# Kernel tuning notes

Measured on AMD Instinct MI355X. Metric: run time of the kernel, lower is better.

The kernel has to match this reference:

```python
import jax, jax.numpy as jnp
import numpy as np

EPS = 1e-3
D_MODEL = 512
SEQ = 1024
BATCH = 4
N_LAYERS = 2
N_HEAD = 8
D_HEAD = 64
D_INNER = 1024


def _position_table(n_pos, d):
    # Faithful to PositionEncoding: sin applied to even cols; the cos line in
    # the source is a no-op (missing assignment), so odd cols stay raw.
    j = np.arange(d)
    pos = np.arange(n_pos)[:, None]
    pe = pos / np.power(10000.0, 2 * (j // 2) / d)
    pe[0] = 0.0
    pe[1:, 0::2] = np.sin(pe[1:, 0::2])
    return jnp.asarray(pe, dtype=jnp.float32)


def _layer_norm(z, a, b):
    # torch.std is unbiased (ddof=1); eps added to sigma, not variance
    mu = jnp.mean(z, axis=-1, keepdims=True)
    sigma = jnp.sqrt(jnp.sum((z - mu) ** 2, axis=-1, keepdims=True) / (z.shape[-1] - 1))
    return (z - mu) / (sigma + EPS) * a + b


def setup_inputs() -> dict:
    key = jax.random.key(0)
    ks = jax.random.split(key, 10)
    s = 0.02
    return {
        "x": jax.random.normal(ks[0], (BATCH, SEQ, D_MODEL), dtype=jnp.float32),
        "pos_enc": _position_table(SEQ, D_MODEL),
        "w_qs": jax.random.normal(ks[1], (N_LAYERS, N_HEAD, D_MODEL, D_HEAD), dtype=jnp.float32) * s,
        "w_ks": jax.random.normal(ks[2], (N_LAYERS, N_HEAD, D_MODEL, D_HEAD), dtype=jnp.float32) * s,
        "w_vs": jax.random.normal(ks[3], (N_LAYERS, N_HEAD, D_MODEL, D_HEAD), dtype=jnp.float32) * s,
        "ln1_a": jnp.ones((N_LAYERS, D_MODEL), dtype=jnp.float32),
        "ln1_b": jnp.zeros((N_LAYERS, D_MODEL), dtype=jnp.float32),
        "w1": jax.random.normal(ks[4], (N_LAYERS, D_INNER, D_MODEL), dtype=jnp.float32) * s,
        "b1": jax.random.normal(ks[5], (N_LAYERS, D_INNER), dtype=jnp.float32) * s,
        "w2": jax.random.normal(ks[6], (N_LAYERS, D_MODEL, D_INNER), dtype=jnp.float32) * s,
        "b2": jax.random.normal(ks[7], (N_LAYERS, D_MODEL), dtype=jnp.float32) * s,
        "ln2_a": jnp.ones((N_LAYERS, D_MODEL), dtype=jnp.float32),
        "ln2_b": jnp.zeros((N_LAYERS, D_MODEL), dtype=jnp.float32),
    }


def reference(x, pos_enc, w_qs, w_ks, w_vs, ln1_a, ln1_b, w1, b1, w2, b2, ln2_a, ln2_b):
    temper = jnp.sqrt(jnp.float32(D_MODEL))  # scale uses d_model, not d_k (as in source)
    x = x + pos_enc[None, :, :]
    for i in range(N_LAYERS):
        residual = x
        # per-head projections: [h, b, l, dk]
        q = jnp.einsum('bld,hdk->hblk', x, w_qs[i])
        k = jnp.einsum('bld,hdk->hblk', x, w_ks[i])
        v = jnp.einsum('bld,hdv->hblv', x, w_vs[i])
        attn = jax.nn.softmax(jnp.einsum('hbqk,hbmk->hbqm', q, k) / temper, axis=-1)
        out = jnp.einsum('hbqm,hbmv->hbqv', attn, v)
        # permute(1,2,0,3): concat heads along feature dim -> [b, l, h*dv]
        out = out.transpose(1, 2, 0, 3).reshape(BATCH, SEQ, N_HEAD * D_HEAD)
        x = _layer_norm(out + residual, ln1_a[i], ln1_b[i])
        # positionwise FFN (1x1 convs == linears)
        h = jax.nn.relu(jnp.einsum('bld,fd->blf', x, w1[i]) + b1[i])
        o = jnp.einsum('blf,df->bld', h, w2[i]) + b2[i]
        x = _layer_norm(o + x, ln2_a[i], ln2_b[i])
    return x
```

## Files before the change

kernel.cpp:

```cpp
#include <hip/hip_runtime.h>
#include <math.h>

#define D_MODEL 512
#define SEQ     1024
#define BATCH   4
#define N_LAYERS 2
#define N_HEAD  8
#define D_HEAD  64
#define D_INNER 1024
#define NTOK    (BATCH*SEQ)
#define LN_EPS  1e-3f

typedef float f32x4 __attribute__((ext_vector_type(4)));
typedef short bf16x8 __attribute__((ext_vector_type(8)));
typedef unsigned short ushort_t;
typedef unsigned int uint_t;
typedef unsigned long long ull_t;

__device__ inline ushort_t f2bf(float f) {
    uint_t u = __float_as_uint(f);
    u += 0x7FFFu + ((u >> 16) & 1u);
    return (ushort_t)(u >> 16);
}
__device__ inline float bf2f(ushort_t h) {
    return __uint_as_float((uint_t)h << 16);
}

#define PREP_E0 (NTOK * D_MODEL)
#define PREP_E1 (1536 * 512)
#define PREP_EW (N_LAYERS * D_INNER * D_MODEL)
#define PREP_TOTAL (PREP_E0 + 2 * PREP_E1 + 2 * PREP_EW)

__global__ void prep_kernel(const float* __restrict__ x,
                            const float* __restrict__ pe,
                            const float* __restrict__ w_qs,
                            const float* __restrict__ w_ks,
                            const float* __restrict__ w_vs,
                            const float* __restrict__ w1,
                            const float* __restrict__ w2,
                            float* __restrict__ X,
                            ushort_t* __restrict__ Xraw,
                            ushort_t* __restrict__ Wqkv,
                            ushort_t* __restrict__ WqkvL,
                            ushort_t* __restrict__ W1b,
                            ushort_t* __restrict__ W2b) {
    int idx = blockIdx.x * 256 + threadIdx.x;
    if (idx < PREP_E0) {
        int l = (idx / D_MODEL) % SEQ;
        int d = idx % D_MODEL;
        float xv = x[idx];
        X[idx] = xv + pe[l * D_MODEL + d];
        Xraw[idx] = f2bf(xv);
        return;
    }
    idx -= PREP_E0;
    if (idx < 2 * PREP_E1) {
        int layer = idx / PREP_E1;
        int j = idx - layer * PREP_E1;
        int n = j >> 9, k = j & 511;
        int which = n >> 9, h = (n >> 6) & 7, d = n & 63;
        size_t wofs = (size_t)layer * N_HEAD * D_MODEL * D_HEAD;
        const float* W = (which == 0) ? w_qs + wofs
                       : (which == 1) ? w_ks + wofs : w_vs + wofs;
        float v = W[((size_t)h * D_MODEL + k) * D_HEAD + d];
        ushort_t hv = f2bf(v);
        Wqkv[(size_t)layer * PREP_E1 + j] = hv;
        if (layer == 0) WqkvL[j] = f2bf(v - bf2f(hv));
        return;
    }
    idx -= 2 * PREP_E1;
    if (idx < PREP_EW) { W1b[idx] = f2bf(w1[idx]); return; }
    idx -= PREP_EW;
    W2b[idx] = f2bf(w2[idx]);
}

__device__ inline void qkv_scatter(f32x4 a, int n, int m_base,
                                   const float* __restrict__ pew,
                                   ushort_t* Qhi, ushort_t* Qlo,
                                   ushort_t* Khi, ushort_t* Klo,
                                   ushort_t* Vt) {
    int which = n >> 9, hd = n & 511;
    int head = hd >> 6, d = hd & 63;
    int hb = head * BATCH + (m_base >> 10);
    int l  = m_base & 1023;
    if (pew) {
#pragma unroll
        for (int r = 0; r < 4; r++) a[r] += pew[(size_t)(l + r) * 1536 + n];
    }
    if (which == 2) {
        ushort4 pk = make_ushort4(f2bf(a[0]), f2bf(a[1]), f2bf(a[2]), f2bf(a[3]));
        *(ushort4*)(Vt + ((size_t)hb * D_HEAD + d) * SEQ + l) = pk;
    } else {
        ushort_t* H = (which == 0) ? Qhi : Khi;
        ushort_t* L = (which == 0) ? Qlo : Klo;
#pragma unroll
        for (int r = 0; r < 4; r++) {
            float v = a[r];
            ushort_t hv = f2bf(v);
            size_t off = ((size_t)hb * SEQ + l + r) * D_HEAD + d;
            H[off] = hv;
            L[off] = f2bf(v - bf2f(hv));
        }
    }
}

template<int MODE, int TM, int TN, int BK>
__global__ __launch_bounds__(256, 4)
void gemm_kernel(const ushort_t* __restrict__ A, const ushort_t* __restrict__ Bt,
                 const float* __restrict__ bias, const float* __restrict__ pew,
                 float* __restrict__ outF, ushort_t* __restrict__ outB,
                 ushort_t* __restrict__ Qhi, ushort_t* __restrict__ Qlo,
                 ushort_t* __restrict__ Khi, ushort_t* __restrict__ Klo,
                 ushort_t* __restrict__ Vt,
                 int M, int N, int K) {
    constexpr int WM = TM / 2, WN = TN / 2;
    constexpr int MT = WM / 16, NT = WN / 16;
    constexpr int CPR = BK / 8;
    __shared__ ushort_t As[TM][BK + 8];
    __shared__ ushort_t Bs[TN][BK + 8];
    const int tid = threadIdx.x;
    const int m0 = blockIdx.y * TM, n0 = blockIdx.x * TN;
    const int w = tid >> 6, lane = tid & 63;
    const int wr = w >> 1, wc = w & 1;
    const int col = lane & 15, quad = lane >> 4;

    f32x4 acc[MT][NT] = {};

    for (int k0 = 0; k0 < K; k0 += BK) {
        __syncthreads();
#pragma unroll
        for (int p = 0; p < TM * CPR / 256; p++) {
            int idx = p * 256 + tid;
            int row = idx / CPR, ch = (idx % CPR) * 8;
            *(uint4*)(&As[row][ch]) =
                *(const uint4*)(A + (size_t)(m0 + row) * K + k0 + ch);
        }
#pragma unroll
        for (int p = 0; p < TN * CPR / 256; p++) {
            int idx = p * 256 + tid;
            int row = idx / CPR, ch = (idx % CPR) * 8;
            *(uint4*)(&Bs[row][ch]) =
                *(const uint4*)(Bt + (size_t)(n0 + row) * K + k0 + ch);
        }
        __syncthreads();
#pragma unroll
        for (int ks = 0; ks < BK; ks += 32) {
            bf16x8 af[MT], bfr[NT];
#pragma unroll
            for (int t = 0; t < MT; t++)
                af[t] = *(const bf16x8*)(&As[wr * WM + t * 16 + col][ks + quad * 8]);
#pragma unroll
            for (int t = 0; t < NT; t++)
                bfr[t] = *(const bf16x8*)(&Bs[wc * WN + t * 16 + col][ks + quad * 8]);
#pragma unroll
            for (int mt = 0; mt < MT; mt++)
#pragma unroll
                for (int nt = 0; nt < NT; nt++)
                    acc[mt][nt] = __builtin_amdgcn_mfma_f32_16x16x32_bf16(
                        af[mt], bfr[nt], acc[mt][nt], 0, 0, 0);
        }
    }

#pragma unroll
    for (int mt = 0; mt < MT; mt++) {
#pragma unroll
        for (int nt = 0; nt < NT; nt++) {
            int n = n0 + wc * WN + nt * 16 + col;
            int m_base = m0 + wr * WM + mt * 16 + quad * 4;
            if (MODE == 0) {
                qkv_scatter(acc[mt][nt], n, m_base, pew, Qhi, Qlo, Khi, Klo, Vt);
            } else {
#pragma unroll
                for (int r = 0; r < 4; r++) {
                    int m = m_base + r;
                    float v = acc[mt][nt][r];
                    if (MODE == 1) {
                        float t = fmaxf(v + bias[n], 0.f);
                        outB[(size_t)m * N + n] = f2bf(t);
                    } else {
                        outF[(size_t)m * N + n] = v + bias[n];
                    }
                }
            }
        }
    }
}

__global__ __launch_bounds__(256, 4)
void gemm_hilo_kernel(const float* __restrict__ A,
                      const ushort_t* __restrict__ Bh,
                      const ushort_t* __restrict__ Bl,
                      float* __restrict__ outF, int M, int N, int K) {
    __shared__ ushort_t Ash[64][72];
    __shared__ ushort_t Asl[64][72];
    __shared__ ushort_t Bsh[64][72];
    __shared__ ushort_t Bsl[64][72];
    const int tid = threadIdx.x;
    const int m0 = blockIdx.y * 64, n0 = blockIdx.x * 64;
    const int w = tid >> 6, lane = tid & 63;
    const int wm = (w >> 1) * 32, wn = (w & 1) * 32;
    const int col = lane & 15, quad = lane >> 4;

    f32x4 acc[2][2] = {};

    for (int k0 = 0; k0 < K; k0 += 64) {
        __syncthreads();
#pragma unroll
        for (int p = 0; p < 4; p++) {
            int idx = p * 256 + tid;
            int row = idx >> 4, c4 = (idx & 15) * 4;
            float4 v = *(const float4*)(A + (size_t)(m0 + row) * K + k0 + c4);
            ushort_t h0 = f2bf(v.x), h1 = f2bf(v.y), h2 = f2bf(v.z), h3 = f2bf(v.w);
            *(ushort4*)(&Ash[row][c4]) = make_ushort4(h0, h1, h2, h3);
            *(ushort4*)(&Asl[row][c4]) = make_ushort4(
                f2bf(v.x - bf2f(h0)), f2bf(v.y - bf2f(h1)),
                f2bf(v.z - bf2f(h2)), f2bf(v.w - bf2f(h3)));
        }
#pragma unroll
        for (int p = 0; p < 2; p++) {
            int idx = p * 256 + tid;
            int row = idx >> 3, ch = (idx & 7) * 8;
            *(uint4*)(&Bsh[row][ch]) =
                *(const uint4*)(Bh + (size_t)(n0 + row) * K + k0 + ch);
            *(uint4*)(&Bsl[row][ch]) =
                *(const uint4*)(Bl + (size_t)(n0 + row) * K + k0 + ch);
        }
        __syncthreads();
#pragma unroll
        for (int ks = 0; ks < 64; ks += 32) {
            bf16x8 ah[2], al[2], bh[2], bl[2];
#pragma unroll
            for (int t = 0; t < 2; t++) {
                ah[t] = *(const bf16x8*)(&Ash[wm + t * 16 + col][ks + quad * 8]);
                al[t] = *(const bf16x8*)(&Asl[wm + t * 16 + col][ks + quad * 8]);
                bh[t] = *(const bf16x8*)(&Bsh[wn + t * 16 + col][ks + quad * 8]);
                bl[t] = *(const bf16x8*)(&Bsl[wn + t * 16 + col][ks + quad * 8]);
            }
#pragma unroll
            for (int mt = 0; mt < 2; mt++)
#pragma unroll
                for (int nt = 0; nt < 2; nt++) {
                    acc[mt][nt] = __builtin_amdgcn_mfma_f32_16x16x32_bf16(
                        ah[mt], bh[nt], acc[mt][nt], 0, 0, 0);
                    acc[mt][nt] = __builtin_amdgcn_mfma_f32_16x16x32_bf16(
                        ah[mt], bl[nt], acc[mt][nt], 0, 0, 0);
                    acc[mt][nt] = __builtin_amdgcn_mfma_f32_16x16x32_bf16(
                        al[mt], bh[nt], acc[mt][nt], 0, 0, 0);
                }
        }
    }

#pragma unroll
    for (int mt = 0; mt < 2; mt++)
#pragma unroll
        for (int nt = 0; nt < 2; nt++) {
            int n = n0 + wn + nt * 16 + col;
#pragma unroll
            for (int r = 0; r < 4; r++) {
                int m = m0 + wm + mt * 16 + quad * 4 + r;
                outF[(size_t)m * N + n] = acc[mt][nt][r];
            }
        }
}

template<bool HILO>
__global__ __launch_bounds__(256, 2)
void attention_kernel(const ushort_t* __restrict__ Qhi,
                      const ushort_t* __restrict__ Qlo,
                      const ushort_t* __restrict__ Khi,
                      const ushort_t* __restrict__ Klo,
                      const ushort_t* __restrict__ Vt,
                      float* __restrict__ O) {
    const int bid = blockIdx.x;
    const int j   = bid >> 3;
    const int hb  = (bid & 7) * 4 + (j >> 4);
    const int qt  = j & 15;
    const int h = hb >> 2, b = hb & 3;
    const int tid = threadIdx.x;
    const int w = tid >> 6, lane = tid & 63;
    const int col = lane & 15, quad = lane >> 4;
    const size_t kbase = (size_t)hb * SEQ * D_HEAD;
    const size_t vbase = (size_t)hb * D_HEAD * SEQ;

    __shared__ ushort_t Kh[128][72];
    __shared__ ushort_t Kl[HILO ? 128 : 1][72];
    __shared__ ushort_t Vs[64][136];
    __shared__ ushort_t Pl[4][16][68];

    bf16x8 qh[2], ql[2];
    {
        const ushort_t* qp = Qhi + kbase + (size_t)(qt * 64 + w * 16 + col) * D_HEAD;
        qh[0] = *(const bf16x8*)(qp + quad * 8);
        qh[1] = *(const bf16x8*)(qp + 32 + quad * 8);
        if (HILO) {
            const ushort_t* lp = Qlo + kbase + (size_t)(qt * 64 + w * 16 + col) * D_HEAD;
            ql[0] = *(const bf16x8*)(lp + quad * 8);
            ql[1] = *(const bf16x8*)(lp + 32 + quad * 8);
        }
    }

    f32x4 acco[4] = {};
    float mrun[4], lrun[4];
#pragma unroll
    for (int r = 0; r < 4; r++) { mrun[r] = -1e30f; lrun[r] = 0.f; }
    const float inv_temper = 0.04419417382415922f;

    for (int t0 = 0; t0 < SEQ; t0 += 128) {
        __syncthreads();
#pragma unroll
        for (int p = 0; p < 4; p++) {
            int idx = p * 256 + tid;
            int row = idx >> 3, ch = (idx & 7) * 8;
            *(uint4*)(&Kh[row][ch]) =
                *(const uint4*)(Khi + kbase + (size_t)(t0 + row) * D_HEAD + ch);
            if (HILO)
                *(uint4*)(&Kl[row][ch]) =
                    *(const uint4*)(Klo + kbase + (size_t)(t0 + row) * D_HEAD + ch);
        }
#pragma unroll
        for (int p = 0; p < 4; p++) {
            int idx = p * 256 + tid;
            int row = idx >> 4, ch = (idx & 15) * 8;
            *(uint4*)(&Vs[row][ch]) =
                *(const uint4*)(Vt + vbase + (size_t)row * SEQ + t0 + ch);
        }
        __syncthreads();

#pragma unroll
        for (int st = 0; st < 2; st++) {
            const int ko = st * 64;

            float sc[4][4];
#pragma unroll
            for (int nt = 0; nt < 4; nt++) {
                bf16x8 bh0 = *(const bf16x8*)(&Kh[ko + nt * 16 + col][quad * 8]);
                bf16x8 bh1 = *(const bf16x8*)(&Kh[ko + nt * 16 + col][32 + quad * 8]);
                f32x4 s = {};
                s = __builtin_amdgcn_mfma_f32_16x16x32_bf16(qh[0], bh0, s, 0, 0, 0);
                s = __builtin_amdgcn_mfma_f32_16x16x32_bf16(qh[1], bh1, s, 0, 0, 0);
                if (HILO) {
                    bf16x8 bl0 = *(const bf16x8*)(&Kl[ko + nt * 16 + col][quad * 8]);
                    bf16x8 bl1 = *(const bf16x8*)(&Kl[ko + nt * 16 + col][32 + quad * 8]);
                    s = __builtin_amdgcn_mfma_f32_16x16x32_bf16(qh[0], bl0, s, 0, 0, 0);
                    s = __builtin_amdgcn_mfma_f32_16x16x32_bf16(qh[1], bl1, s, 0, 0, 0);
                    s = __builtin_amdgcn_mfma_f32_16x16x32_bf16(ql[0], bh0, s, 0, 0, 0);
                    s = __builtin_amdgcn_mfma_f32_16x16x32_bf16(ql[1], bh1, s, 0, 0, 0);
                }
#pragma unroll
                for (int r = 0; r < 4; r++) sc[nt][r] = s[r] * inv_temper;
            }

            float tmax[4];
#pragma unroll
            for (int r = 0; r < 4; r++)
                tmax[r] = fmaxf(fmaxf(sc[0][r], sc[1][r]), fmaxf(sc[2][r], sc[3][r]));
#pragma unroll
            for (int mask = 1; mask < 16; mask <<= 1)
#pragma unroll
                for (int r = 0; r < 4; r++)
                    tmax[r] = fmaxf(tmax[r], __shfl_xor(tmax[r], mask, 64));

            float alpha[4], tsum[4];
#pragma unroll
            for (int r = 0; r < 4; r++) {
                float mn = fmaxf(mrun[r], tmax[r]);
                alpha[r] = __expf(mrun[r] - mn);
                mrun[r] = mn;
                tsum[r] = 0.f;
            }
#pragma unroll
            for (int nt = 0; nt < 4; nt++)
#pragma unroll
                for (int r = 0; r < 4; r++) {
                    float pv = __expf(sc[nt][r] - mrun[r]);
                    tsum[r] += pv;
                    Pl[w][quad * 4 + r][nt * 16 + col] = f2bf(pv);
                }
#pragma unroll
            for (int mask = 1; mask < 16; mask <<= 1)
#pragma unroll
                for (int r = 0; r < 4; r++)
                    tsum[r] += __shfl_xor(tsum[r], mask, 64);
#pragma unroll
            for (int r = 0; r < 4; r++)
                lrun[r] = lrun[r] * alpha[r] + tsum[r];
#pragma unroll
            for (int nt = 0; nt < 4; nt++)
#pragma unroll
                for (int r = 0; r < 4; r++)
                    acco[nt][r] *= alpha[r];

            __threadfence_block();

            union { ulong2 u; bf16x8 v; } a0, a1;
            a0.u.x = *(const ull_t*)(&Pl[w][col][quad * 8]);
            a0.u.y = *(const ull_t*)(&Pl[w][col][quad * 8 + 4]);
            a1.u.x = *(const ull_t*)(&Pl[w][col][32 + quad * 8]);
            a1.u.y = *(const ull_t*)(&Pl[w][col][32 + quad * 8 + 4]);
#pragma unroll
            for (int nt = 0; nt < 4; nt++) {
                bf16x8 bv0 = *(const bf16x8*)(&Vs[nt * 16 + col][ko + quad * 8]);
                bf16x8 bv1 = *(const bf16x8*)(&Vs[nt * 16 + col][ko + 32 + quad * 8]);
                acco[nt] = __builtin_amdgcn_mfma_f32_16x16x32_bf16(a0.v, bv0, acco[nt], 0, 0, 0);
                acco[nt] = __builtin_amdgcn_mfma_f32_16x16x32_bf16(a1.v, bv1, acco[nt], 0, 0, 0);
            }
        }
    }

#pragma unroll
    for (int nt = 0; nt < 4; nt++) {
#pragma unroll
        for (int r = 0; r < 4; r++) {
            int row = qt * 64 + w * 16 + quad * 4 + r;
            O[((size_t)b * SEQ + row) * D_MODEL + h * D_HEAD + nt * 16 + col]
                = acco[nt][r] / lrun[r];
        }
    }
}

__device__ inline float block_sum_256(float v, float* tmp) {
#pragma unroll
    for (int off = 32; off > 0; off >>= 1) v += __shfl_down(v, off, 64);
    if ((threadIdx.x & 63) == 0) tmp[threadIdx.x >> 6] = v;
    __syncthreads();
    return tmp[0] + tmp[1] + tmp[2] + tmp[3];
}

__global__ void add_norm_kernel(const float* __restrict__ A,
                                const float* __restrict__ R,
                                const float* __restrict__ ga,
                                const float* __restrict__ gb,
                                float* __restrict__ Out,
                                ushort_t* __restrict__ OutBf) {
    int tok = blockIdx.x, tid = threadIdx.x;
    __shared__ float t1[4], t2[4];
    size_t base = (size_t)tok * D_MODEL;
    float z0 = A[base + tid]       + R[base + tid];
    float z1 = A[base + tid + 256] + R[base + tid + 256];
    float s = block_sum_256(z0 + z1, t1);
    float mu = s * (1.f / (float)D_MODEL);
    float d0 = z0 - mu, d1 = z1 - mu;
    float ss = block_sum_256(d0 * d0 + d1 * d1, t2);
    float sigma = sqrtf(ss * (1.f / (float)(D_MODEL - 1)));
    float inv = 1.f / (sigma + LN_EPS);
    float r0 = d0 * inv * ga[tid]       + gb[tid];
    float r1 = d1 * inv * ga[tid + 256] + gb[tid + 256];
    Out[base + tid]         = r0;
    Out[base + tid + 256]   = r1;
    OutBf[base + tid]       = f2bf(r0);
    OutBf[base + tid + 256] = f2bf(r1);
}

extern "C" void kernel_launch(void* const* d_in, const int* in_sizes, int n_in,
                              void* d_out, int out_size, void* d_ws, size_t ws_size,
                              hipStream_t stream) {
    const float* x     = (const float*)d_in[0];
    const float* pe    = (const float*)d_in[1];
    const float* w_qs  = (const float*)d_in[2];
    const float* w_ks  = (const float*)d_in[3];
    const float* w_vs  = (const float*)d_in[4];
    const float* ln1_a = (const float*)d_in[5];
    const float* ln1_b = (const float*)d_in[6];
    const float* w1    = (const float*)d_in[7];
    const float* b1    = (const float*)d_in[8];
    const float* w2    = (const float*)d_in[9];
    const float* b2    = (const float*)d_in[10];
    const float* ln2_a = (const float*)d_in[11];
    const float* ln2_b = (const float*)d_in[12];
    float* out = (float*)d_out;

    const size_t NXD = (size_t)NTOK * D_MODEL;
    char* p = (char*)d_ws;
    float*    X    = (float*)p;     p += NXD * 4;
    float*    Ob   = (float*)p;     p += NXD * 4;
    ushort_t* Xbf  = (ushort_t*)p;  p += NXD * 2;
    ushort_t* Xraw = (ushort_t*)p;  p += NXD * 2;
    ushort_t* Qhi  = (ushort_t*)p;  p += NXD * 2;
    ushort_t* Qlo  = (ushort_t*)p;  p += NXD * 2;
    ushort_t* Khi  = (ushort_t*)p;  p += NXD * 2;
    ushort_t* Klo  = (ushort_t*)p;  p += NXD * 2;
    ushort_t* Vt   = (ushort_t*)p;  p += NXD * 2;
    ushort_t* Wqkv = (ushort_t*)p;  p += (size_t)N_LAYERS * 1536 * 512 * 2;
    ushort_t* WqkvL= (ushort_t*)p;  p += (size_t)1536 * 512 * 2;
    ushort_t* W1b  = (ushort_t*)p;  p += (size_t)N_LAYERS * D_INNER * D_MODEL * 2;
    ushort_t* W2b  = (ushort_t*)p;
    ushort_t* Hbf  = Qhi;
    float*    PEW  = Ob;

    prep_kernel<<<(PREP_TOTAL + 255) / 256, 256, 0, stream>>>(
        x, pe, w_qs, w_ks, w_vs, w1, w2, X, Xraw, Wqkv, WqkvL, W1b, W2b);

    for (int i = 0; i < N_LAYERS; i++) {
        if (i == 0) {
            gemm_hilo_kernel<<<dim3(1536 / 64, SEQ / 64), 256, 0, stream>>>(
                pe, Wqkv, WqkvL, PEW, SEQ, 1536, D_MODEL);
            gemm_kernel<0, 64, 64, 128><<<dim3(1536 / 64, NTOK / 64), 256, 0, stream>>>(
                Xraw, Wqkv, nullptr, PEW, nullptr, nullptr,
                Qhi, Qlo, Khi, Klo, Vt, NTOK, 1536, D_MODEL);
            attention_kernel<true><<<512, 256, 0, stream>>>(
                Qhi, Qlo, Khi, Klo, Vt, Ob);
        } else {
            gemm_kernel<0, 64, 64, 128><<<dim3(1536 / 64, NTOK / 64), 256, 0, stream>>>(
                Xbf, Wqkv + (size_t)i * 1536 * 512, nullptr, nullptr, nullptr,
                nullptr, Qhi, Qlo, Khi, Klo, Vt, NTOK, 1536, D_MODEL);
            attention_kernel<false><<<512, 256, 0, stream>>>(
                Qhi, Qlo, Khi, Klo, Vt, Ob);
        }

        add_norm_kernel<<<NTOK, 256, 0, stream>>>(
            Ob, X, ln1_a + i * D_MODEL, ln1_b + i * D_MODEL, X, Xbf);

        gemm_kernel<1, 64, 64, 128><<<dim3(D_INNER / 64, NTOK / 64), 256, 0, stream>>>(
            Xbf, W1b + (size_t)i * D_INNER * D_MODEL, b1 + (size_t)i * D_INNER,
            nullptr, nullptr, Hbf, nullptr, nullptr, nullptr, nullptr, nullptr,
            NTOK, D_INNER, D_MODEL);

        gemm_kernel<2, 64, 64, 128><<<dim3(D_MODEL / 64, NTOK / 64), 256, 0, stream>>>(
            Hbf, W2b + (size_t)i * D_MODEL * D_INNER, b2 + (size_t)i * D_MODEL,
            nullptr, Ob, nullptr, nullptr, nullptr, nullptr, nullptr, nullptr,
            NTOK, D_MODEL, D_INNER);

        float* dst = (i == N_LAYERS - 1) ? out : X;
        add_norm_kernel<<<NTOK, 256, 0, stream>>>(
            Ob, X, ln2_a + i * D_MODEL, ln2_b + i * D_MODEL, dst, Xbf);
    }
}
```

Baseline: 301.9 us.

## Split attention KV range in two, drop LDS staging, combine in add-norm

The attention kernel now splits each query tile's key range into two halves across 1024 blocks and writes unnormalized partial outputs plus per-row max and sum. An add-norm combine kernel merges the two halves and applies layer norm. K and V fragments are now read directly from global memory instead of being staged through shared memory, and the operands are transposed so each lane owns one query row, which simplifies the softmax reductions. The aim is more parallelism and occupancy (launch bounds raised to 4), at the cost of extra partial-output traffic and uncoalesced, unshared global loads of K and V.

```diff
diff --git a/kernel.cpp b/kernel.cpp
--- a/kernel.cpp
+++ b/kernel.cpp
@@ -264,16 +264,20 @@
 }
 
 template<bool HILO>
-__global__ __launch_bounds__(256, 2)
+__global__ __launch_bounds__(256, 4)
 void attention_kernel(const ushort_t* __restrict__ Qhi,
                       const ushort_t* __restrict__ Qlo,
                       const ushort_t* __restrict__ Khi,
                       const ushort_t* __restrict__ Klo,
                       const ushort_t* __restrict__ Vt,
-                      float* __restrict__ O) {
+                      float* __restrict__ P0,
+                      float* __restrict__ P1,
+                      float2* __restrict__ ML) {
     const int bid = blockIdx.x;
-    const int j   = bid >> 3;
-    const int hb  = (bid & 7) * 4 + (j >> 4);
+    const int split = bid >> 9;
+    const int r9  = bid & 511;
+    const int j   = r9 >> 3;
+    const int hb  = (r9 & 7) * 4 + (j >> 4);
     const int qt  = j & 15;
     const int h = hb >> 2, b = hb & 3;
     const int tid = threadIdx.x;
@@ -282,10 +286,7 @@
     const size_t kbase = (size_t)hb * SEQ * D_HEAD;
     const size_t vbase = (size_t)hb * D_HEAD * SEQ;
 
-    __shared__ ushort_t Kh[128][72];
-    __shared__ ushort_t Kl[HILO ? 128 : 1][72];
-    __shared__ ushort_t Vs[64][136];
-    __shared__ ushort_t Pl[4][16][68];
+    __shared__ ushort_t Pl[4][16][72];
 
     bf16x8 qh[2], ql[2];
     {
@@ -300,122 +301,92 @@
     }
 
     f32x4 acco[4] = {};
-    float mrun[4], lrun[4];
-#pragma unroll
-    for (int r = 0; r < 4; r++) { mrun[r] = -1e30f; lrun[r] = 0.f; }
+    float mrun = -1e30f, lrun = 0.f;
     const float inv_temper = 0.04419417382415922f;
 
-    for (int t0 = 0; t0 < SEQ; t0 += 128) {
-        __syncthreads();
-#pragma unroll
-        for (int p = 0; p < 4; p++) {
-            int idx = p * 256 + tid;
-            int row = idx >> 3, ch = (idx & 7) * 8;
-            *(uint4*)(&Kh[row][ch]) =
-                *(const uint4*)(Khi + kbase + (size_t)(t0 + row) * D_HEAD + ch);
-            if (HILO)
-                *(uint4*)(&Kl[row][ch]) =
-                    *(const uint4*)(Klo + kbase + (size_t)(t0 + row) * D_HEAD + ch);
-        }
-#pragma unroll
-        for (int p = 0; p < 4; p++) {
-            int idx = p * 256 + tid;
-            int row = idx >> 4, ch = (idx & 15) * 8;
-            *(uint4*)(&Vs[row][ch]) =
-                *(const uint4*)(Vt + vbase + (size_t)row * SEQ + t0 + ch);
-        }
-        __syncthreads();
-
-#pragma unroll
-        for (int st = 0; st < 2; st++) {
-            const int ko = st * 64;
-
-            float sc[4][4];
-#pragma unroll
-            for (int nt = 0; nt < 4; nt++) {
-                bf16x8 bh0 = *(const bf16x8*)(&Kh[ko + nt * 16 + col][quad * 8]);
-                bf16x8 bh1 = *(const bf16x8*)(&Kh[ko + nt * 16 + col][32 + quad * 8]);
-                f32x4 s = {};
-                s = __builtin_amdgcn_mfma_f32_16x16x32_bf16(qh[0], bh0, s, 0, 0, 0);
-                s = __builtin_amdgcn_mfma_f32_16x16x32_bf16(qh[1], bh1, s, 0, 0, 0);
-                if (HILO) {
-                    bf16x8 bl0 = *(const bf16x8*)(&Kl[ko + nt * 16 + col][quad * 8]);
-                    bf16x8 bl1 = *(const bf16x8*)(&Kl[ko + nt * 16 + col][32 + quad * 8]);
-                    s = __builtin_amdgcn_mfma_f32_16x16x32_bf16(qh[0], bl0, s, 0, 0, 0);
-                    s = __builtin_amdgcn_mfma_f32_16x16x32_bf16(qh[1], bl1, s, 0, 0, 0);
-                    s = __builtin_amdgcn_mfma_f32_16x16x32_bf16(ql[0], bh0, s, 0, 0, 0);
-                    s = __builtin_amdgcn_mfma_f32_16x16x32_bf16(ql[1], bh1, s, 0, 0, 0);
-                }
-#pragma unroll
-                for (int r = 0; r < 4; r++) sc[nt][r] = s[r] * inv_temper;
+    const int tbeg = split * (SEQ / 2);
+    for (int t0 = tbeg; t0 < tbeg + SEQ / 2; t0 += 64) {
+        float sc[4][4];
+#pragma unroll
+        for (int nt = 0; nt < 4; nt++) {
+            const ushort_t* kp = Khi + kbase + (size_t)(t0 + nt * 16 + col) * D_HEAD;
+            bf16x8 kh0 = *(const bf16x8*)(kp + quad * 8);
+            bf16x8 kh1 = *(const bf16x8*)(kp + 32 + quad * 8);
+            f32x4 s = {};
+            s = __builtin_amdgcn_mfma_f32_16x16x32_bf16(kh0, qh[0], s, 0, 0, 0);
+            s = __builtin_amdgcn_mfma_f32_16x16x32_bf16(kh1, qh[1], s, 0, 0, 0);
+            if (HILO) {
+                const ushort_t* lp2 = Klo + kbase + (size_t)(t0 + nt * 16 + col) * D_HEAD;
+                bf16x8 kl0 = *(const bf16x8*)(lp2 + quad * 8);
+                bf16x8 kl1 = *(const bf16x8*)(lp2 + 32 + quad * 8);
+                s = __builtin_amdgcn_mfma_f32_16x16x32_bf16(kl0, qh[0], s, 0, 0, 0);
+                s = __builtin_amdgcn_mfma_f32_16x16x32_bf16(kl1, qh[1], s, 0, 0, 0);
+                s = __builtin_amdgcn_mfma_f32_16x16x32_bf16(kh0, ql[0], s, 0, 0, 0);
+                s = __builtin_amdgcn_mfma_f32_16x16x32_bf16(kh1, ql[1], s, 0, 0, 0);
             }
-
-            float tmax[4];
-#pragma unroll
-            for (int r = 0; r < 4; r++)
-                tmax[r] = fmaxf(fmaxf(sc[0][r], sc[1][r]), fmaxf(sc[2][r], sc[3][r]));
-#pragma unroll
-            for (int mask = 1; mask < 16; mask <<= 1)
-#pragma unroll
-                for (int r = 0; r < 4; r++)
-                    tmax[r] = fmaxf(tmax[r], __shfl_xor(tmax[r], mask, 64));
-
-            float alpha[4], tsum[4];
-#pragma unroll
-            for (int r = 0; r < 4; r++) {
-                float mn = fmaxf(mrun[r], tmax[r]);
-                alpha[r] = __expf(mrun[r] - mn);
-                mrun[r] = mn;
-                tsum[r] = 0.f;
-            }
-#pragma unroll
-            for (int nt = 0; nt < 4; nt++)
-#pragma unroll
-                for (int r = 0; r < 4; r++) {
-                    float pv = __expf(sc[nt][r] - mrun[r]);
-                    tsum[r] += pv;
-                    Pl[w][quad * 4 + r][nt * 16 + col] = f2bf(pv);
-                }
-#pragma unroll
-            for (int mask = 1; mask < 16; mask <<= 1)
-#pragma unroll
-                for (int r = 0; r < 4; r++)
-                    tsum[r] += __shfl_xor(tsum[r], mask, 64);
-#pragma unroll
-            for (int r = 0; r < 4; r++)
-                lrun[r] = lrun[r] * alpha[r] + tsum[r];
-#pragma unroll
-            for (int nt = 0; nt < 4; nt++)
-#pragma unroll
-                for (int r = 0; r < 4; r++)
-                    acco[nt][r] *= alpha[r];
-
-            __threadfence_block();
-
-            union { ulong2 u; bf16x8 v; } a0, a1;
-            a0.u.x = *(const ull_t*)(&Pl[w][col][quad * 8]);
-            a0.u.y = *(const ull_t*)(&Pl[w][col][quad * 8 + 4]);
-            a1.u.x = *(const ull_t*)(&Pl[w][col][32 + quad * 8]);
-            a1.u.y = *(const ull_t*)(&Pl[w][col][32 + quad * 8 + 4]);
-#pragma unroll
-            for (int nt = 0; nt < 4; nt++) {
-                bf16x8 bv0 = *(const bf16x8*)(&Vs[nt * 16 + col][ko + quad * 8]);
-                bf16x8 bv1 = *(const bf16x8*)(&Vs[nt * 16 + col][ko + 32 + quad * 8]);
-                acco[nt] = __builtin_amdgcn_mfma_f32_16x16x32_bf16(a0.v, bv0, acco[nt], 0, 0, 0);
-                acco[nt] = __builtin_amdgcn_mfma_f32_16x16x32_bf16(a1.v, bv1, acco[nt], 0, 0, 0);
-            }
-        }
-    }
-
-#pragma unroll
-    for (int nt = 0; nt < 4; nt++) {
-#pragma unroll
-        for (int r = 0; r < 4; r++) {
-            int row = qt * 64 + w * 16 + quad * 4 + r;
-            O[((size_t)b * SEQ + row) * D_MODEL + h * D_HEAD + nt * 16 + col]
-                = acco[nt][r] / lrun[r];
-        }
-    }
+#pragma unroll
+            for (int r = 0; r < 4; r++) sc[nt][r] = s[r] * inv_temper;
+        }
+
+        bf16x8 va0[4], va1[4];
+#pragma unroll
+        for (int nt = 0; nt < 4; nt++) {
+            const ushort_t* vp = Vt + vbase + (size_t)(nt * 16 + col) * SEQ + t0;
+            va0[nt] = *(const bf16x8*)(vp + quad * 8);
+            va1[nt] = *(const bf16x8*)(vp + 32 + quad * 8);
+        }
+
+        float tmax = sc[0][0];
+#pragma unroll
+        for (int nt = 0; nt < 4; nt++)
+#pragma unroll
+            for (int r = 0; r < 4; r++) tmax = fmaxf(tmax, sc[nt][r]);
+        tmax = fmaxf(tmax, __shfl_xor(tmax, 16, 64));
+        tmax = fmaxf(tmax, __shfl_xor(tmax, 32, 64));
+
+        float mn = fmaxf(mrun, tmax);
+        float alpha = __expf(mrun - mn);
+        mrun = mn;
+        float tsum = 0.f;
+#pragma unroll
+        for (int nt = 0; nt < 4; nt++) {
+            float p0 = __expf(sc[nt][0] - mn);
+            float p1 = __expf(sc[nt][1] - mn);
+            float p2 = __expf(sc[nt][2] - mn);
+            float p3 = __expf(sc[nt][3] - mn);
+            tsum += (p0 + p1) + (p2 + p3);
+            ull_t pk = (ull_t)f2bf(p0) | ((ull_t)f2bf(p1) << 16)
+                     | ((ull_t)f2bf(p2) << 32) | ((ull_t)f2bf(p3) << 48);
+            *(ull_t*)(&Pl[w][col][nt * 16 + quad * 4]) = pk;
+        }
+        tsum += __shfl_xor(tsum, 16, 64);
+        tsum += __shfl_xor(tsum, 32, 64);
+        lrun = lrun * alpha + tsum;
+#pragma unroll
+        for (int nt = 0; nt < 4; nt++)
+#pragma unroll
+            for (int r = 0; r < 4; r++) acco[nt][r] *= alpha;
+
+        __threadfence_block();
+
+        union { ulong2 u; bf16x8 v; } pa0, pa1;
+        pa0.u = *(const ulong2*)(&Pl[w][col][quad * 8]);
+        pa1.u = *(const ulong2*)(&Pl[w][col][32 + quad * 8]);
+#pragma unroll
+        for (int nt = 0; nt < 4; nt++) {
+            acco[nt] = __builtin_amdgcn_mfma_f32_16x16x32_bf16(va0[nt], pa0.v, acco[nt], 0, 0, 0);
+            acco[nt] = __builtin_amdgcn_mfma_f32_16x16x32_bf16(va1[nt], pa1.v, acco[nt], 0, 0, 0);
+        }
+    }
+
+    const int qrow = qt * 64 + w * 16 + col;
+    float* dst = split ? P1 : P0;
+#pragma unroll
+    for (int nt = 0; nt < 4; nt++)
+        *(f32x4*)(&dst[((size_t)b * SEQ + qrow) * D_MODEL + h * D_HEAD
+                       + nt * 16 + quad * 4]) = acco[nt];
+    if (quad == 0)
+        ML[((size_t)split * 32 + hb) * SEQ + qrow] = make_float2(mrun, lrun);
 }
 
 __device__ inline float block_sum_256(float v, float* tmp) {
@@ -451,6 +422,53 @@
     OutBf[base + tid + 256] = f2bf(r1);
 }
 
+__global__ void add_norm_combine_kernel(const float* __restrict__ Pa,
+                                        const float* __restrict__ Pb,
+                                        const float2* __restrict__ ML,
+                                        const float* __restrict__ R,
+                                        const float* __restrict__ ga,
+                                        const float* __restrict__ gb,
+                                        float* __restrict__ Out,
+                                        ushort_t* __restrict__ OutBf) {
+    int tok = blockIdx.x, tid = threadIdx.x;
+    int b = tok >> 10, l = tok & 1023;
+    __shared__ float t1[4], t2[4];
+    int h0 = tid >> 6;
+    float s0a, s0b, s1a, s1b;
+    {
+        int hb0 = h0 * 4 + b;
+        float2 u0 = ML[(size_t)hb0 * SEQ + l];
+        float2 u1 = ML[(size_t)(32 + hb0) * SEQ + l];
+        float M = fmaxf(u0.x, u1.x);
+        float e0 = __expf(u0.x - M), e1 = __expf(u1.x - M);
+        float inv = 1.f / (e0 * u0.y + e1 * u1.y);
+        s0a = e0 * inv; s0b = e1 * inv;
+        int hb1 = (h0 + 4) * 4 + b;
+        float2 v0 = ML[(size_t)hb1 * SEQ + l];
+        float2 v1 = ML[(size_t)(32 + hb1) * SEQ + l];
+        float M2 = fmaxf(v0.x, v1.x);
+        float f0 = __expf(v0.x - M2), f1 = __expf(v1.x - M2);
+        float inv2 = 1.f / (f0 * v0.y + f1 * v1.y);
+        s1a = f0 * inv2; s1b = f1 * inv2;
+    }
+    size_t base = (size_t)tok * D_MODEL;
+    float z0 = Pa[base + tid] * s0a + Pb[base + tid] * s0b + R[base + tid];
+    float z1 = Pa[base + tid + 256] * s1a + Pb[base + tid + 256] * s1b
+             + R[base + tid + 256];
+    float s = block_sum_256(z0 + z1, t1);
+    float mu = s * (1.f / (float)D_MODEL);
+    float d0 = z0 - mu, d1 = z1 - mu;
+    float ss = block_sum_256(d0 * d0 + d1 * d1, t2);
+    float sigma = sqrtf(ss * (1.f / (float)(D_MODEL - 1)));
+    float inv = 1.f / (sigma + LN_EPS);
+    float r0 = d0 * inv * ga[tid]       + gb[tid];
+    float r1 = d1 * inv * ga[tid + 256] + gb[tid + 256];
+    Out[base + tid]         = r0;
+    Out[base + tid + 256]   = r1;
+    OutBf[base + tid]       = f2bf(r0);
+    OutBf[base + tid + 256] = f2bf(r1);
+}
+
 extern "C" void kernel_launch(void* const* d_in, const int* in_sizes, int n_in,
                               void* d_out, int out_size, void* d_ws, size_t ws_size,
                               hipStream_t stream) {
@@ -483,7 +501,8 @@
     ushort_t* Wqkv = (ushort_t*)p;  p += (size_t)N_LAYERS * 1536 * 512 * 2;
     ushort_t* WqkvL= (ushort_t*)p;  p += (size_t)1536 * 512 * 2;
     ushort_t* W1b  = (ushort_t*)p;  p += (size_t)N_LAYERS * D_INNER * D_MODEL * 2;
-    ushort_t* W2b  = (ushort_t*)p;
+    ushort_t* W2b  = (ushort_t*)p;  p += (size_t)N_LAYERS * D_MODEL * D_INNER * 2;
+    float2*   ML   = (float2*)p;
     ushort_t* Hbf  = Qhi;
     float*    PEW  = Ob;
 
@@ -497,18 +516,18 @@
             gemm_kernel<0, 64, 64, 128><<<dim3(1536 / 64, NTOK / 64), 256, 0, stream>>>(
                 Xraw, Wqkv, nullptr, PEW, nullptr, nullptr,
                 Qhi, Qlo, Khi, Klo, Vt, NTOK, 1536, D_MODEL);
-            attention_kernel<true><<<512, 256, 0, stream>>>(
-                Qhi, Qlo, Khi, Klo, Vt, Ob);
+            attention_kernel<true><<<1024, 256, 0, stream>>>(
+                Qhi, Qlo, Khi, Klo, Vt, Ob, out, ML);
         } else {
             gemm_kernel<0, 64, 64, 128><<<dim3(1536 / 64, NTOK / 64), 256, 0, stream>>>(
                 Xbf, Wqkv + (size_t)i * 1536 * 512, nullptr, nullptr, nullptr,
                 nullptr, Qhi, Qlo, Khi, Klo, Vt, NTOK, 1536, D_MODEL);
-            attention_kernel<false><<<512, 256, 0, stream>>>(
-                Qhi, Qlo, Khi, Klo, Vt, Ob);
-        }
-
-        add_norm_kernel<<<NTOK, 256, 0, stream>>>(
-            Ob, X, ln1_a + i * D_MODEL, ln1_b + i * D_MODEL, X, Xbf);
+            attention_kernel<false><<<1024, 256, 0, stream>>>(
+                Qhi, Qlo, Khi, Klo, Vt, Ob, out, ML);
+        }
+
+        add_norm_combine_kernel<<<NTOK, 256, 0, stream>>>(
+            Ob, out, ML, X, ln1_a + i * D_MODEL, ln1_b + i * D_MODEL, X, Xbf);
 
         gemm_kernel<1, 64, 64, 128><<<dim3(D_INNER / 64, NTOK / 64), 256, 0, stream>>>(
             Xbf, W1b + (size_t)i * D_INNER * D_MODEL, b1 + (size_t)i * D_INNER,
```

Result: slower. 378.1 us (+25.2%).
